# Performance work log

Hardware: AMD Instinct MI355X
Metric: run time of the kernel (lower is better)

Reference implementation:

```python
import jax, jax.numpy as jnp
import numpy as np


def sign_fn(x):
    # torch.sign(torch.sign(x) + 0.5): maps x >= 0 -> +1, x < 0 -> -1 (zero -> +1)
    return jnp.where(x >= 0, 1.0, -1.0).astype(x.dtype)


def setup_inputs() -> dict:
    key = jax.random.key(0)
    kx, kw, kb = jax.random.split(key, 3)
    TOKENS, IN, OUT = 8192, 4096, 4096
    x = jax.random.normal(kx, (TOKENS, IN), dtype=jnp.float32)
    weight = jax.random.normal(kw, (OUT, IN), dtype=jnp.float32)
    bias = jax.random.normal(kb, (OUT,), dtype=jnp.float32)
    return {"x": x, "weight": weight, "bias": bias}


def reference(x, weight, bias):
    b_weight = sign_fn(weight)  # [out, in], values in {+1, -1}
    b_bias = sign_fn(bias)      # [out]
    # nn.functional.linear: y = x @ W^T + b
    return jnp.einsum('ti,oi->to', x, b_weight) + b_bias
```

## Files before the change

### kernel.cpp

```cpp
#include <hip/hip_runtime.h>


typedef __attribute__((ext_vector_type(4))) int   i32x4;
typedef __attribute__((ext_vector_type(8))) short short8;
typedef __attribute__((ext_vector_type(4))) float f32x4;

constexpr int M = 8192;
constexpr int N = 4096;
constexpr int K = 4096;

constexpr int BM = 256, BN = 256, BK = 64;
constexpr int NTILES = K / BK;
constexpr int TILE_A = BM * BK;
constexpr int TILE_B = BN * BK;
constexpr int BUFSZ  = TILE_A + TILE_B;
constexpr int RING   = 4;

__device__ __forceinline__ void load_lds16(const void* g, void* l) {
    __builtin_amdgcn_global_load_lds(
        (const __attribute__((address_space(1))) unsigned int*)g,
        (__attribute__((address_space(3))) unsigned int*)l, 16, 0, 0);
}

__global__ __launch_bounds__(256) void prep_fused(
    const float* __restrict__ X, const float* __restrict__ W,
    signed char* __restrict__ Xq, signed char* __restrict__ Wq,
    float* __restrict__ Scale) {
    __shared__ float wmax[4];
    const int t = threadIdx.x;

    if (blockIdx.x < M) {
        const int row = blockIdx.x;
        const float4* xr = reinterpret_cast<const float4*>(X + (size_t)row * K);
        float4 v[4];
        float mx = 0.f;
#pragma unroll
        for (int i = 0; i < 4; ++i) {
            v[i] = xr[t + i * 256];
            mx = fmaxf(mx, fmaxf(fmaxf(fabsf(v[i].x), fabsf(v[i].y)),
                                 fmaxf(fabsf(v[i].z), fabsf(v[i].w))));
        }
#pragma unroll
        for (int off = 32; off > 0; off >>= 1)
            mx = fmaxf(mx, __shfl_down(mx, off));
        if ((t & 63) == 0) wmax[t >> 6] = mx;
        __syncthreads();
        float rmax = fmaxf(fmaxf(wmax[0], wmax[1]), fmaxf(wmax[2], wmax[3]));
        rmax = fmaxf(rmax, 1e-20f);
        const float inv = 127.f / rmax;
        if (t == 0) Scale[row] = rmax * (1.f / 127.f);

        unsigned int* out = reinterpret_cast<unsigned int*>(Xq + (size_t)row * K);
#pragma unroll
        for (int i = 0; i < 4; ++i) {
            int q0 = (int)rintf(v[i].x * inv);
            int q1 = (int)rintf(v[i].y * inv);
            int q2 = (int)rintf(v[i].z * inv);
            int q3 = (int)rintf(v[i].w * inv);
            unsigned int p = (q0 & 255) | ((q1 & 255) << 8) |
                             ((q2 & 255) << 16) | ((unsigned)(q3 & 255) << 24);
            out[t + i * 256] = p;
        }
    } else {
        size_t i = (size_t)(blockIdx.x - M) * 256 + t;
        const float4* s = reinterpret_cast<const float4*>(W) + i * 2;
        float4 a = s[0], b = s[1];
        auto sg = [](float f) -> unsigned int { return (f >= 0.f) ? 1u : 0xFFu; };
        uint2 o;
        o.x = sg(a.x) | (sg(a.y) << 8) | (sg(a.z) << 16) | (sg(a.w) << 24);
        o.y = sg(b.x) | (sg(b.y) << 8) | (sg(b.z) << 16) | (sg(b.w) << 24);
        reinterpret_cast<uint2*>(Wq)[i] = o;
    }
}

template <int VMN>
__device__ __forceinline__ void kstep(const signed char* smem, int t,
                                      int wm, int wn, int rl, int cq16,
                                      i32x4 (&acc)[8][4]) {
    asm volatile("s_waitcnt vmcnt(%0)" :: "i"(VMN) : "memory");
    __builtin_amdgcn_s_barrier();
    asm volatile("" ::: "memory");

    const signed char* Ab = smem + (t & (RING - 1)) * BUFSZ;
    const signed char* Bb = Ab + TILE_A;
    i32x4 a[8], b[4];
#pragma unroll
    for (int mi = 0; mi < 8; ++mi)
        a[mi] = *reinterpret_cast<const i32x4*>(
            Ab + (wm * 128 + mi * 16 + rl) * BK + cq16);
#pragma unroll
    for (int ni = 0; ni < 4; ++ni)
        b[ni] = *reinterpret_cast<const i32x4*>(
            Bb + (wn * 64 + ni * 16 + rl) * BK + cq16);

    __builtin_amdgcn_s_setprio(1);
#pragma unroll
    for (int mi = 0; mi < 8; ++mi)
#pragma unroll
        for (int ni = 0; ni < 4; ++ni)
            acc[mi][ni] = __builtin_amdgcn_mfma_i32_16x16x64_i8(
                a[mi], b[ni], acc[mi][ni], 0, 0, 0);
    __builtin_amdgcn_s_setprio(0);

    asm volatile("" ::: "memory");
    __builtin_amdgcn_s_barrier();
}

__global__ __launch_bounds__(512, 2) void gemm_i8_p(
    const signed char* __restrict__ Aq, const signed char* __restrict__ Bq,
    const float* __restrict__ Scale, const float* __restrict__ Bias,
    float* __restrict__ OUT) {
    __shared__ signed char smem[RING * BUFSZ];

    const int tid  = threadIdx.x;
    const int lane = tid & 63;
    const int w    = tid >> 6;
    const int wm   = w >> 2;
    const int wn   = w & 3;
    const int rl   = lane & 15;
    const int cq16 = (((lane >> 4) ^ ((rl >> 1) & 3)) << 4);

    const int wg  = blockIdx.x;
    const int lin = (wg & 7) * 64 + (wg >> 3);
    const int n0  = (lin & 15) * BN;
    const int m0  = (lin >> 4) * BM;

    const int srow = tid >> 2;
    const int cg   = ((tid & 3) ^ ((srow >> 1) & 3)) * 16;
    const signed char* gA0 = Aq + (size_t)(m0 + srow)       * K + cg;
    const signed char* gA1 = Aq + (size_t)(m0 + 128 + srow) * K + cg;
    const signed char* gB0 = Bq + (size_t)(n0 + srow)       * K + cg;
    const signed char* gB1 = Bq + (size_t)(n0 + 128 + srow) * K + cg;
    signed char* lbase = smem + w * 1024;

    auto stage = [&](int t) {
        signed char* d = lbase + (t & (RING - 1)) * BUFSZ;
        const size_t ko = (size_t)t * BK;
        load_lds16(gA0 + ko, d);
        load_lds16(gA1 + ko, d + 8192);
        load_lds16(gB0 + ko, d + TILE_A);
        load_lds16(gB1 + ko, d + TILE_A + 8192);
    };

    i32x4 acc[8][4];
#pragma unroll
    for (int mi = 0; mi < 8; ++mi)
#pragma unroll
        for (int ni = 0; ni < 4; ++ni)
            acc[mi][ni] = (i32x4){0, 0, 0, 0};

    stage(0); stage(1); stage(2);

    int t = 0;
    for (; t < NTILES - 3; ++t) {
        stage(t + 3);
        kstep<12>(smem, t, wm, wn, rl, cq16, acc);
    }
    kstep<8>(smem, t, wm, wn, rl, cq16, acc); ++t;
    kstep<4>(smem, t, wm, wn, rl, cq16, acc); ++t;
    kstep<0>(smem, t, wm, wn, rl, cq16, acc);

#pragma unroll
    for (int ni = 0; ni < 4; ++ni) {
        const int gcol = n0 + wn * 64 + ni * 16 + rl;
        const float sb = (Bias[gcol] >= 0.f) ? 1.f : -1.f;
#pragma unroll
        for (int mi = 0; mi < 8; ++mi) {
            const int growb = m0 + wm * 128 + mi * 16 + (lane >> 4) * 4;
            const float4 sc = *reinterpret_cast<const float4*>(&Scale[growb]);
            OUT[(size_t)(growb + 0) * N + gcol] = (float)acc[mi][ni][0] * sc.x + sb;
            OUT[(size_t)(growb + 1) * N + gcol] = (float)acc[mi][ni][1] * sc.y + sb;
            OUT[(size_t)(growb + 2) * N + gcol] = (float)acc[mi][ni][2] * sc.z + sb;
            OUT[(size_t)(growb + 3) * N + gcol] = (float)acc[mi][ni][3] * sc.w + sb;
        }
    }
}

constexpr int MT   = 128;
constexpr int NTF  = 128;
constexpr int LDSS = 40;
constexpr int KTB  = 32;
__device__ __forceinline__ unsigned short f2b(float f) {
    unsigned int u = __builtin_bit_cast(unsigned int, f);
    u += 0x7FFFu + ((u >> 16) & 1u);
    return (unsigned short)(u >> 16);
}
__global__ __launch_bounds__(256) void binlin_fallback(
    const float* __restrict__ X, const float* __restrict__ W,
    const float* __restrict__ B, float* __restrict__ OUT) {
    __shared__ unsigned short As[MT][LDSS];
    __shared__ unsigned short Bs[NTF][LDSS];
    const int tid  = threadIdx.x;
    const int lane = tid & 63;
    const int wave = tid >> 6;
    const int wm   = wave >> 1;
    const int wn   = wave & 1;
    const int m0 = blockIdx.y * MT;
    const int n0 = blockIdx.x * NTF;
    const int rl = lane & 15;
    const int kq = (lane >> 4) * 8;
    f32x4 acc[4][4];
#pragma unroll
    for (int mi = 0; mi < 4; ++mi)
#pragma unroll
        for (int ni = 0; ni < 4; ++ni)
            acc[mi][ni] = (f32x4){0.f, 0.f, 0.f, 0.f};
    for (int k0 = 0; k0 < K; k0 += KTB) {
#pragma unroll
        for (int it = 0; it < 4; ++it) {
            int g = tid + it * 256, row = g >> 3, c4 = (g & 7) << 2;
            float4 v = *reinterpret_cast<const float4*>(&X[(size_t)(m0 + row) * K + k0 + c4]);
            ushort4 h;
            h.x = f2b(v.x); h.y = f2b(v.y); h.z = f2b(v.z); h.w = f2b(v.w);
            *reinterpret_cast<ushort4*>(&As[row][c4]) = h;
        }
#pragma unroll
        for (int it = 0; it < 4; ++it) {
            int g = tid + it * 256, row = g >> 3, c4 = (g & 7) << 2;
            float4 v = *reinterpret_cast<const float4*>(&W[(size_t)(n0 + row) * K + k0 + c4]);
            ushort4 h;
            h.x = (v.x >= 0.f) ? 0x3F80u : 0xBF80u;
            h.y = (v.y >= 0.f) ? 0x3F80u : 0xBF80u;
            h.z = (v.z >= 0.f) ? 0x3F80u : 0xBF80u;
            h.w = (v.w >= 0.f) ? 0x3F80u : 0xBF80u;
            *reinterpret_cast<ushort4*>(&Bs[row][c4]) = h;
        }
        __syncthreads();
        short8 a[4], b[4];
#pragma unroll
        for (int mi = 0; mi < 4; ++mi)
            a[mi] = *reinterpret_cast<const short8*>(&As[wm * 64 + mi * 16 + rl][kq]);
#pragma unroll
        for (int ni = 0; ni < 4; ++ni)
            b[ni] = *reinterpret_cast<const short8*>(&Bs[wn * 64 + ni * 16 + rl][kq]);
#pragma unroll
        for (int mi = 0; mi < 4; ++mi)
#pragma unroll
            for (int ni = 0; ni < 4; ++ni)
                acc[mi][ni] = __builtin_amdgcn_mfma_f32_16x16x32_bf16(
                    a[mi], b[ni], acc[mi][ni], 0, 0, 0);
        __syncthreads();
    }
#pragma unroll
    for (int ni = 0; ni < 4; ++ni) {
        int gcol = n0 + wn * 64 + ni * 16 + rl;
        float sb = (B[gcol] >= 0.f) ? 1.f : -1.f;
#pragma unroll
        for (int mi = 0; mi < 4; ++mi) {
            int growb = m0 + wm * 64 + mi * 16 + (lane >> 4) * 4;
#pragma unroll
            for (int r = 0; r < 4; ++r)
                OUT[(size_t)(growb + r) * N + gcol] = acc[mi][ni][r] + sb;
        }
    }
}

extern "C" void kernel_launch(void* const* d_in, const int* in_sizes, int n_in,
                              void* d_out, int out_size, void* d_ws, size_t ws_size,
                              hipStream_t stream) {
    const float* x  = (const float*)d_in[0];
    const float* w  = (const float*)d_in[1];
    const float* b  = (const float*)d_in[2];
    float* out      = (float*)d_out;

    const size_t need = (size_t)M * K + (size_t)N * K + (size_t)M * sizeof(float);
    if (ws_size >= need) {
        signed char* Xq = (signed char*)d_ws;
        signed char* Wq = Xq + (size_t)M * K;
        float* Scale    = (float*)(Wq + (size_t)N * K);

        const unsigned prepw_blocks = (unsigned)((size_t)N * K / 8 / 256);
        prep_fused<<<dim3(M + prepw_blocks), dim3(256), 0, stream>>>(x, w, Xq, Wq, Scale);

        gemm_i8_p<<<dim3((M / BM) * (N / BN)), dim3(512), 0, stream>>>(
            Xq, Wq, Scale, b, out);
    } else {
        dim3 grid(N / NTF, M / MT);
        binlin_fallback<<<grid, dim3(256), 0, stream>>>(x, w, b, out);
    }
}
```

Before: 404.6 us.

## Interleave LDS loads, global prefetch and MFMA in four phases; wave-per-row prep

The GEMM main loop now splits each K-step into four phases. Each phase loads two A fragments from LDS, issues one quarter of the next tile's global-to-LDS copies and runs eight MFMAs, which keeps far fewer A registers live and spreads memory traffic across the compute. The prep kernel now quantizes one activation row per wave, with no LDS reduction or block sync, and writes 16-byte stores. The weight-sign part uses a fixed grid-stride loop of 1024 blocks. The cost is more barriers per K-step and a careful vmcnt accounting that must stay correct.

After: 403.2 us. Within noise of the previous version (-0.3%).

```diff
diff --git a/kernel.cpp b/kernel.cpp
--- a/kernel.cpp
+++ b/kernel.cpp
@@ -22,88 +22,138 @@
         (__attribute__((address_space(3))) unsigned int*)l, 16, 0, 0);
 }
 
+constexpr int XB = M / 4;
+constexpr int WB = 1024;
+constexpr int WCH = N * K / 8;
+
 __global__ __launch_bounds__(256) void prep_fused(
     const float* __restrict__ X, const float* __restrict__ W,
     signed char* __restrict__ Xq, signed char* __restrict__ Wq,
     float* __restrict__ Scale) {
-    __shared__ float wmax[4];
-    const int t = threadIdx.x;
-
-    if (blockIdx.x < M) {
-        const int row = blockIdx.x;
+    const int t    = threadIdx.x;
+    const int lane = t & 63;
+    const int wv   = t >> 6;
+
+    if (blockIdx.x < XB) {
+        const int row = blockIdx.x * 4 + wv;
         const float4* xr = reinterpret_cast<const float4*>(X + (size_t)row * K);
-        float4 v[4];
+        float4 v[16];
         float mx = 0.f;
 #pragma unroll
         for (int i = 0; i < 4; ++i) {
-            v[i] = xr[t + i * 256];
-            mx = fmaxf(mx, fmaxf(fmaxf(fabsf(v[i].x), fabsf(v[i].y)),
-                                 fmaxf(fabsf(v[i].z), fabsf(v[i].w))));
+#pragma unroll
+            for (int j = 0; j < 4; ++j) {
+                float4 f = xr[4 * lane + 256 * i + j];
+                v[4 * i + j] = f;
+                mx = fmaxf(mx, fmaxf(fmaxf(fabsf(f.x), fabsf(f.y)),
+                                     fmaxf(fabsf(f.z), fabsf(f.w))));
+            }
         }
 #pragma unroll
         for (int off = 32; off > 0; off >>= 1)
             mx = fmaxf(mx, __shfl_down(mx, off));
-        if ((t & 63) == 0) wmax[t >> 6] = mx;
-        __syncthreads();
-        float rmax = fmaxf(fmaxf(wmax[0], wmax[1]), fmaxf(wmax[2], wmax[3]));
-        rmax = fmaxf(rmax, 1e-20f);
-        const float inv = 127.f / rmax;
-        if (t == 0) Scale[row] = rmax * (1.f / 127.f);
-
-        unsigned int* out = reinterpret_cast<unsigned int*>(Xq + (size_t)row * K);
+        mx = __shfl(mx, 0);
+        const float rmax = fmaxf(mx, 1e-20f);
+        const float inv  = 127.f / rmax;
+        if (lane == 0) Scale[row] = rmax * (1.f / 127.f);
+
+        uint4* out4 = reinterpret_cast<uint4*>(Xq + (size_t)row * K);
 #pragma unroll
         for (int i = 0; i < 4; ++i) {
-            int q0 = (int)rintf(v[i].x * inv);
-            int q1 = (int)rintf(v[i].y * inv);
-            int q2 = (int)rintf(v[i].z * inv);
-            int q3 = (int)rintf(v[i].w * inv);
-            unsigned int p = (q0 & 255) | ((q1 & 255) << 8) |
-                             ((q2 & 255) << 16) | ((unsigned)(q3 & 255) << 24);
-            out[t + i * 256] = p;
+            uint4 o;
+            unsigned int* op = &o.x;
+#pragma unroll
+            for (int j = 0; j < 4; ++j) {
+                float4 f = v[4 * i + j];
+                int q0 = (int)rintf(f.x * inv);
+                int q1 = (int)rintf(f.y * inv);
+                int q2 = (int)rintf(f.z * inv);
+                int q3 = (int)rintf(f.w * inv);
+                op[j] = (q0 & 255) | ((q1 & 255) << 8) |
+                        ((q2 & 255) << 16) | ((unsigned)(q3 & 255) << 24);
+            }
+            out4[lane + 64 * i] = o;
         }
     } else {
-        size_t i = (size_t)(blockIdx.x - M) * 256 + t;
-        const float4* s = reinterpret_cast<const float4*>(W) + i * 2;
-        float4 a = s[0], b = s[1];
+        const float4* W4 = reinterpret_cast<const float4*>(W);
+        uint2* O = reinterpret_cast<uint2*>(Wq);
         auto sg = [](float f) -> unsigned int { return (f >= 0.f) ? 1u : 0xFFu; };
-        uint2 o;
-        o.x = sg(a.x) | (sg(a.y) << 8) | (sg(a.z) << 16) | (sg(a.w) << 24);
-        o.y = sg(b.x) | (sg(b.y) << 8) | (sg(b.z) << 16) | (sg(b.w) << 24);
-        reinterpret_cast<uint2*>(Wq)[i] = o;
-    }
-}
-
-template <int VMN>
-__device__ __forceinline__ void kstep(const signed char* smem, int t,
-                                      int wm, int wn, int rl, int cq16,
-                                      i32x4 (&acc)[8][4]) {
-    asm volatile("s_waitcnt vmcnt(%0)" :: "i"(VMN) : "memory");
+        size_t idx = (size_t)(blockIdx.x - XB) * 256 + t;
+        const size_t stride = (size_t)WB * 256;
+        for (size_t c = idx; c < (size_t)WCH; c += stride) {
+            float4 a = W4[c * 2], b = W4[c * 2 + 1];
+            uint2 o;
+            o.x = sg(a.x) | (sg(a.y) << 8) | (sg(a.z) << 16) | (sg(a.w) << 24);
+            o.y = sg(b.x) | (sg(b.y) << 8) | (sg(b.z) << 16) | (sg(b.w) << 24);
+            O[c] = o;
+        }
+    }
+}
+
+struct GemmCtx {
+    const signed char* gA0;
+    const signed char* gA1;
+    const signed char* gB0;
+    const signed char* gB1;
+    signed char* lbase;
+    int wm, wn, rl, cq16;
+};
+
+template <int P, bool STAGE>
+__device__ __forceinline__ void phase(
+    const GemmCtx& c, const signed char* Ab, const signed char* Bb,
+    signed char* dst, size_t ko,
+    i32x4 (&a)[2], i32x4 (&b)[4], i32x4 (&acc)[8][4]) {
+    if constexpr (P == 0) {
+#pragma unroll
+        for (int ni = 0; ni < 4; ++ni)
+            b[ni] = *reinterpret_cast<const i32x4*>(
+                Bb + (c.wn * 64 + ni * 16 + c.rl) * BK + c.cq16);
+    }
+    a[0] = *reinterpret_cast<const i32x4*>(
+        Ab + (c.wm * 128 + (2 * P + 0) * 16 + c.rl) * BK + c.cq16);
+    a[1] = *reinterpret_cast<const i32x4*>(
+        Ab + (c.wm * 128 + (2 * P + 1) * 16 + c.rl) * BK + c.cq16);
+    if constexpr (STAGE) {
+        if constexpr (P == 0) load_lds16(c.gA0 + ko, dst);
+        if constexpr (P == 1) load_lds16(c.gA1 + ko, dst + 8192);
+        if constexpr (P == 2) load_lds16(c.gB0 + ko, dst + TILE_A);
+        if constexpr (P == 3) load_lds16(c.gB1 + ko, dst + TILE_A + 8192);
+    }
+    asm volatile("" ::: "memory");
     __builtin_amdgcn_s_barrier();
+    asm volatile("s_waitcnt lgkmcnt(0)" ::: "memory");
+    __builtin_amdgcn_sched_barrier(0);
+    __builtin_amdgcn_s_setprio(1);
+#pragma unroll
+    for (int j = 0; j < 2; ++j)
+#pragma unroll
+        for (int ni = 0; ni < 4; ++ni)
+            acc[2 * P + j][ni] = __builtin_amdgcn_mfma_i32_16x16x64_i8(
+                a[j], b[ni], acc[2 * P + j][ni], 0, 0, 0);
+    __builtin_amdgcn_s_setprio(0);
     asm volatile("" ::: "memory");
-
+    if constexpr (P < 3) __builtin_amdgcn_s_barrier();
+}
+
+template <bool STAGE, int VMEND>
+__device__ __forceinline__ void kstep8(
+    const GemmCtx& c, const signed char* smem, int t,
+    i32x4 (&a)[2], i32x4 (&b)[4], i32x4 (&acc)[8][4]) {
     const signed char* Ab = smem + (t & (RING - 1)) * BUFSZ;
     const signed char* Bb = Ab + TILE_A;
-    i32x4 a[8], b[4];
-#pragma unroll
-    for (int mi = 0; mi < 8; ++mi)
-        a[mi] = *reinterpret_cast<const i32x4*>(
-            Ab + (wm * 128 + mi * 16 + rl) * BK + cq16);
-#pragma unroll
-    for (int ni = 0; ni < 4; ++ni)
-        b[ni] = *reinterpret_cast<const i32x4*>(
-            Bb + (wn * 64 + ni * 16 + rl) * BK + cq16);
-
-    __builtin_amdgcn_s_setprio(1);
-#pragma unroll
-    for (int mi = 0; mi < 8; ++mi)
-#pragma unroll
-        for (int ni = 0; ni < 4; ++ni)
-            acc[mi][ni] = __builtin_amdgcn_mfma_i32_16x16x64_i8(
-                a[mi], b[ni], acc[mi][ni], 0, 0, 0);
-    __builtin_amdgcn_s_setprio(0);
-
-    asm volatile("" ::: "memory");
-    __builtin_amdgcn_s_barrier();
+    signed char* dst = c.lbase + ((t + 3) & (RING - 1)) * BUFSZ;
+    const size_t ko = (size_t)(t + 3) * BK;
+
+    phase<0, STAGE>(c, Ab, Bb, dst, ko, a, b, acc);
+    phase<1, STAGE>(c, Ab, Bb, dst, ko, a, b, acc);
+    phase<2, STAGE>(c, Ab, Bb, dst, ko, a, b, acc);
+    phase<3, STAGE>(c, Ab, Bb, dst, ko, a, b, acc);
+    if constexpr (VMEND >= 0) {
+        asm volatile("s_waitcnt vmcnt(%0)" :: "i"(VMEND) : "memory");
+        __builtin_amdgcn_s_barrier();
+        asm volatile("" ::: "memory");
+    }
 }
 
 __global__ __launch_bounds__(512, 2) void gemm_i8_p(
@@ -115,10 +165,11 @@
     const int tid  = threadIdx.x;
     const int lane = tid & 63;
     const int w    = tid >> 6;
-    const int wm   = w >> 2;
-    const int wn   = w & 3;
-    const int rl   = lane & 15;
-    const int cq16 = (((lane >> 4) ^ ((rl >> 1) & 3)) << 4);
+    GemmCtx c;
+    c.wm = w >> 2;
+    c.wn = w & 3;
+    c.rl = lane & 15;
+    c.cq16 = (((lane >> 4) ^ ((c.rl >> 1) & 3)) << 4);
 
     const int wg  = blockIdx.x;
     const int lin = (wg & 7) * 64 + (wg >> 3);
@@ -127,19 +178,19 @@
 
     const int srow = tid >> 2;
     const int cg   = ((tid & 3) ^ ((srow >> 1) & 3)) * 16;
-    const signed char* gA0 = Aq + (size_t)(m0 + srow)       * K + cg;
-    const signed char* gA1 = Aq + (size_t)(m0 + 128 + srow) * K + cg;
-    const signed char* gB0 = Bq + (size_t)(n0 + srow)       * K + cg;
-    const signed char* gB1 = Bq + (size_t)(n0 + 128 + srow) * K + cg;
-    signed char* lbase = smem + w * 1024;
-
-    auto stage = [&](int t) {
-        signed char* d = lbase + (t & (RING - 1)) * BUFSZ;
+    c.gA0 = Aq + (size_t)(m0 + srow)       * K + cg;
+    c.gA1 = Aq + (size_t)(m0 + 128 + srow) * K + cg;
+    c.gB0 = Bq + (size_t)(n0 + srow)       * K + cg;
+    c.gB1 = Bq + (size_t)(n0 + 128 + srow) * K + cg;
+    c.lbase = smem + w * 1024;
+
+    auto stage_full = [&](int t) {
+        signed char* d = c.lbase + (t & (RING - 1)) * BUFSZ;
         const size_t ko = (size_t)t * BK;
-        load_lds16(gA0 + ko, d);
-        load_lds16(gA1 + ko, d + 8192);
-        load_lds16(gB0 + ko, d + TILE_A);
-        load_lds16(gB1 + ko, d + TILE_A + 8192);
+        load_lds16(c.gA0 + ko, d);
+        load_lds16(c.gA1 + ko, d + 8192);
+        load_lds16(c.gB0 + ko, d + TILE_A);
+        load_lds16(c.gB1 + ko, d + TILE_A + 8192);
     };
 
     i32x4 acc[8][4];
@@ -148,25 +199,27 @@
 #pragma unroll
         for (int ni = 0; ni < 4; ++ni)
             acc[mi][ni] = (i32x4){0, 0, 0, 0};
-
-    stage(0); stage(1); stage(2);
+    i32x4 a[2], b[4];
+
+    stage_full(0); stage_full(1); stage_full(2);
+    asm volatile("s_waitcnt vmcnt(8)" ::: "memory");
+    __builtin_amdgcn_s_barrier();
+    asm volatile("" ::: "memory");
 
     int t = 0;
-    for (; t < NTILES - 3; ++t) {
-        stage(t + 3);
-        kstep<12>(smem, t, wm, wn, rl, cq16, acc);
-    }
-    kstep<8>(smem, t, wm, wn, rl, cq16, acc); ++t;
-    kstep<4>(smem, t, wm, wn, rl, cq16, acc); ++t;
-    kstep<0>(smem, t, wm, wn, rl, cq16, acc);
+    for (; t < NTILES - 3; ++t)
+        kstep8<true, 8>(c, smem, t, a, b, acc);
+    kstep8<false, 4>(c, smem, t, a, b, acc); ++t;
+    kstep8<false, 0>(c, smem, t, a, b, acc); ++t;
+    kstep8<false, -1>(c, smem, t, a, b, acc);
 
 #pragma unroll
     for (int ni = 0; ni < 4; ++ni) {
-        const int gcol = n0 + wn * 64 + ni * 16 + rl;
+        const int gcol = n0 + c.wn * 64 + ni * 16 + c.rl;
         const float sb = (Bias[gcol] >= 0.f) ? 1.f : -1.f;
 #pragma unroll
         for (int mi = 0; mi < 8; ++mi) {
-            const int growb = m0 + wm * 128 + mi * 16 + (lane >> 4) * 4;
+            const int growb = m0 + c.wm * 128 + mi * 16 + (lane >> 4) * 4;
             const float4 sc = *reinterpret_cast<const float4*>(&Scale[growb]);
             OUT[(size_t)(growb + 0) * N + gcol] = (float)acc[mi][ni][0] * sc.x + sb;
             OUT[(size_t)(growb + 1) * N + gcol] = (float)acc[mi][ni][1] * sc.y + sb;
@@ -269,9 +322,7 @@
         signed char* Wq = Xq + (size_t)M * K;
         float* Scale    = (float*)(Wq + (size_t)N * K);
 
-        const unsigned prepw_blocks = (unsigned)((size_t)N * K / 8 / 256);
-        prep_fused<<<dim3(M + prepw_blocks), dim3(256), 0, stream>>>(x, w, Xq, Wq, Scale);
-
+        prep_fused<<<dim3(XB + WB), dim3(256), 0, stream>>>(x, w, Xq, Wq, Scale);
         gemm_i8_p<<<dim3((M / BM) * (N / BN)), dim3(512), 0, stream>>>(
             Xq, Wq, Scale, b, out);
     } else {
```
